# Kernel tuning notes

Measured on AMD Instinct MI355X. Metric: run time of the kernel, lower is better.

Reference implementation:

```python
import jax, jax.numpy as jnp
import numpy as np
from jax import lax

# dims
B, T, D = 2, 1024, 512
H, K, V = 8, 64, 64      # head_k_dim = head_v_dim = 64
CONV = 4
# IVON / module hyperparams (from __init__ defaults)
LR, B1, B2, WD, LAM = 1e-3, 0.9, 0.999, 0.0, 1.0
EPS = 1e-5               # RMSNorm eps
SCALE = K ** -0.5


def _silu(x):
    return x * jax.nn.sigmoid(x)


def _short_conv(x, w):
    """Causal depthwise conv1d (kernel_size=CONV, no bias) + SiLU. x:[B,T,C], w:[C,CONV]."""
    xp = jnp.pad(x, ((0, 0), (CONV - 1, 0), (0, 0)))
    y = sum(xp[:, i:i + x.shape[1]] * w[:, i] for i in range(CONV))
    return _silu(y)


def _l2norm(x):
    return x * lax.rsqrt(jnp.sum(x * x, -1, keepdims=True) + 1e-6)


def setup_inputs() -> dict:
    key = jax.random.key(0)
    ks = jax.random.split(key, 10)
    s = 0.02
    return {
        "hidden_states": jax.random.normal(ks[0], (B, T, D), jnp.float32),
        "Wq": jax.random.normal(ks[1], (D, H * K), jnp.float32) * s,
        "Wk": jax.random.normal(ks[2], (D, H * K), jnp.float32) * s,
        "Wv": jax.random.normal(ks[3], (D, H * V), jnp.float32) * s,
        "Wb": jax.random.normal(ks[4], (D, H), jnp.float32) * s,
        "cw_q": jax.random.normal(ks[5], (H * K, CONV), jnp.float32) * 0.5,
        "cw_k": jax.random.normal(ks[6], (H * K, CONV), jnp.float32) * 0.5,
        "cw_v": jax.random.normal(ks[7], (H * V, CONV), jnp.float32) * 0.5,
        "rms_w": jnp.ones((V,), jnp.float32),
        "Wo": jax.random.normal(ks[8], (H * V, D), jnp.float32) * s,
    }


def reference(hidden_states, Wq, Wk, Wv, Wb, cw_q, cw_k, cw_v, rms_w, Wo):
    x = hidden_states
    # projections -> causal depthwise short conv (+SiLU, qk_activation='silu')
    q = _short_conv(x @ Wq, cw_q).reshape(B, T, H, K)
    k = _short_conv(x @ Wk, cw_k).reshape(B, T, H, K)
    v = _short_conv(x @ Wv, cw_v).reshape(B, T, H, V)
    beta = jax.nn.sigmoid(x @ Wb)                     # [B,T,H]
    # qk l2-norm inside kernel (qk_norm='l2'), scale on q
    q = _l2norm(q) * SCALE
    k = _l2norm(k)

    # fused recurrent IVON delta-rule: per-step outer-product gradient of
    # 0.5||k @ S - v||^2, momentum g, diag preconditioner h (noise-free IVON).
    def step(carry, inp):
        S, h, g = carry                               # each [B,H,K,V]
        qt, kt, vt, bt = inp                          # [B,H,K],[B,H,K],[B,H,V],[B,H]
        pred = jnp.einsum('bhk,bhkv->bhv', kt, S)
        grad = kt[..., None] * (pred - vt)[..., None, :]   # [B,H,K,V]
        g = B1 * g + (1.0 - B1) * grad
        h = B2 * h + (1.0 - B2) * grad * grad
        S = S - LR * bt[..., None, None] * (g + WD * S) / (h + LAM)
        o = jnp.einsum('bhk,bhkv->bhv', qt, S)
        return (S, h, g), o

    z = jnp.zeros((B, H, K, V), jnp.float32)
    inps = (jnp.swapaxes(q, 0, 1), jnp.swapaxes(k, 0, 1),
            jnp.swapaxes(v, 0, 1), jnp.swapaxes(beta, 0, 1))
    _, o = lax.scan(step, (z, z, z), inps)            # o: [T,B,H,V]
    o = jnp.swapaxes(o, 0, 1)                          # [B,T,H,V]

    # RMSNorm over head_v_dim, then output projection
    o = o * lax.rsqrt(jnp.mean(o * o, -1, keepdims=True) + EPS) * rms_w
    o = o.reshape(B, T, H * V) @ Wo                    # [B,T,D]
    return o
```

## Files before the change

kernel.cpp:

```cpp
#include <hip/hip_runtime.h>
#include <hip/hip_bf16.h>
#include <math.h>

#define Bb 2
#define Tt 1024
#define Dd 512
#define Hh 8
#define Kk 64
#define Vv 64
#define BT (Bb*Tt)
#define HK (Hh*Kk)

#define B1c 0.9f
#define B2c 0.999f
#define LRc 1e-3f
#define SCALEc 0.125f

typedef short s8v __attribute__((ext_vector_type(8)));
typedef float f4v __attribute__((ext_vector_type(4)));

__device__ __forceinline__ unsigned short f2bf(float x) {
  unsigned u = __float_as_uint(x);
  u += 0x7FFFu + ((u >> 16) & 1u);
  return (unsigned short)(u >> 16);
}
__device__ __forceinline__ float bf2f(unsigned short h) {
  return __uint_as_float((unsigned)h << 16);
}

template <int CTRL>
__device__ __forceinline__ float dpp_add(float v) {
  int y = __builtin_amdgcn_update_dpp(0, __float_as_int(v), CTRL, 0xF, 0xF, true);
  return v + __int_as_float(y);
}

typedef unsigned uint2_t __attribute__((ext_vector_type(2)));

__device__ __forceinline__ float xor16_add(float x) {
#if __has_builtin(__builtin_amdgcn_permlane16_swap)
  uint2_t r = __builtin_amdgcn_permlane16_swap(__float_as_uint(x), __float_as_uint(x),
                                               false, false);
  return __uint_as_float(r.x) + __uint_as_float(r.y);
#else
  int y = __builtin_amdgcn_ds_swizzle(__float_as_int(x), 0x401F);
  return x + __int_as_float(y);
#endif
}

__device__ __forceinline__ float xor32_add(float x) {
#if __has_builtin(__builtin_amdgcn_permlane32_swap)
  uint2_t r = __builtin_amdgcn_permlane32_swap(__float_as_uint(x), __float_as_uint(x),
                                               false, false);
  return __uint_as_float(r.x) + __uint_as_float(r.y);
#else
  return x + __shfl_xor(x, 32, 64);
#endif
}

__device__ __forceinline__ float reduce16(float x) {
  x = dpp_add<0xB1>(x);
  x = dpp_add<0x4E>(x);
  x = dpp_add<0x141>(x);
  x = dpp_add<0x140>(x);
  return x;
}

__device__ __forceinline__ float reduce64(float x) {
  x = reduce16(x);
  x = xor16_add(x);
  x = xor32_add(x);
  return x;
}

__global__ __launch_bounds__(256) void cvt_x_kernel(
    const float* __restrict__ x, unsigned short* __restrict__ hi,
    unsigned short* __restrict__ lo) {
  const int i = (blockIdx.x * 256 + threadIdx.x) * 8;
  float4 a = *(const float4*)(x + i);
  float4 b = *(const float4*)(x + i + 4);
  const float v[8] = {a.x, a.y, a.z, a.w, b.x, b.y, b.z, b.w};
  union { unsigned short u[8]; uint4 q; } ph, pl;
#pragma unroll
  for (int j = 0; j < 8; ++j) {
    unsigned short h = f2bf(v[j]);
    ph.u[j] = h;
    pl.u[j] = f2bf(v[j] - bf2f(h));
  }
  *(uint4*)(hi + i) = ph.q;
  *(uint4*)(lo + i) = pl.q;
}

__global__ __launch_bounds__(256) void cvt_w_kernel(
    const float* __restrict__ W0, const float* __restrict__ W1,
    const float* __restrict__ W2,
    unsigned short* __restrict__ hib, unsigned short* __restrict__ lob) {
  __shared__ float Ts[64][65];
  const int z = blockIdx.z;
  const float* W = (z == 0) ? W0 : (z == 1) ? W1 : W2;
  unsigned short* hi = hib + (size_t)z * 512 * 512;
  unsigned short* lo = lob + (size_t)z * 512 * 512;
  const int tk = blockIdx.x * 64;
  const int tn = blockIdx.y * 64;
  const int r  = threadIdx.x >> 2;
  const int cg = threadIdx.x & 3;
#pragma unroll
  for (int j = 0; j < 4; ++j) {
    float4 v = *(const float4*)(W + (size_t)(tk + r) * 512 + tn + cg * 16 + j * 4);
    Ts[r][cg * 16 + j * 4 + 0] = v.x;
    Ts[r][cg * 16 + j * 4 + 1] = v.y;
    Ts[r][cg * 16 + j * 4 + 2] = v.z;
    Ts[r][cg * 16 + j * 4 + 3] = v.w;
  }
  __syncthreads();
  union { unsigned short u[16]; uint4 q[2]; } ph, pl;
#pragma unroll
  for (int j = 0; j < 16; ++j) {
    float v = Ts[cg * 16 + j][r];
    unsigned short h = f2bf(v);
    ph.u[j] = h;
    pl.u[j] = f2bf(v - bf2f(h));
  }
  const size_t ob = (size_t)(tn + r) * 512 + tk + cg * 16;
  *(uint4*)(hi + ob) = ph.q[0];
  *(uint4*)(hi + ob + 8) = ph.q[1];
  *(uint4*)(lo + ob) = pl.q[0];
  *(uint4*)(lo + ob + 8) = pl.q[1];
}

__device__ __forceinline__ void gemm_mfma_body(
    const unsigned short* __restrict__ Ahi, const unsigned short* __restrict__ Alo,
    const unsigned short* __restrict__ Bhi, const unsigned short* __restrict__ Blo,
    float* __restrict__ C) {
  __shared__ unsigned short Ah[64][40], Al[64][40], Bh[64][40], Bl[64][40];
  const int tid = threadIdx.x;
  const int bm = blockIdx.x * 64;
  const int bn = blockIdx.y * 64;
  const int srow = tid >> 2;
  const int skoff = (tid & 3) * 8;
  const int l = tid & 63, w = tid >> 6;
  const int arow = (l & 15) + 16 * w;
  const int koff = (l >> 4) * 8;

  const unsigned short* pAh = Ahi + (size_t)(bm + srow) * 512 + skoff;
  const unsigned short* pAl = Alo + (size_t)(bm + srow) * 512 + skoff;
  const unsigned short* pBh = Bhi + (size_t)(bn + srow) * 512 + skoff;
  const unsigned short* pBl = Blo + (size_t)(bn + srow) * 512 + skoff;

  f4v acc0 = {0.f, 0.f, 0.f, 0.f}, acc1 = acc0, acc2 = acc0, acc3 = acc0;

  uint4 rah = *(const uint4*)(pAh);
  uint4 ral = *(const uint4*)(pAl);
  uint4 rbh = *(const uint4*)(pBh);
  uint4 rbl = *(const uint4*)(pBl);

  for (int k0 = 0; k0 < 512; k0 += 32) {
    __syncthreads();
    *(uint4*)&Ah[srow][skoff] = rah;
    *(uint4*)&Al[srow][skoff] = ral;
    *(uint4*)&Bh[srow][skoff] = rbh;
    *(uint4*)&Bl[srow][skoff] = rbl;
    __syncthreads();
    if (k0 + 32 < 512) {
      rah = *(const uint4*)(pAh + k0 + 32);
      ral = *(const uint4*)(pAl + k0 + 32);
      rbh = *(const uint4*)(pBh + k0 + 32);
      rbl = *(const uint4*)(pBl + k0 + 32);
    }
    const s8v ah = *(const s8v*)&Ah[arow][koff];
    const s8v al = *(const s8v*)&Al[arow][koff];
#pragma unroll
    for (int c = 0; c < 4; ++c) {
      const s8v bh = *(const s8v*)&Bh[16 * c + (l & 15)][koff];
      const s8v bl = *(const s8v*)&Bl[16 * c + (l & 15)][koff];
      f4v* acc = (c == 0) ? &acc0 : (c == 1) ? &acc1 : (c == 2) ? &acc2 : &acc3;
      *acc = __builtin_amdgcn_mfma_f32_16x16x32_bf16(al, bh, *acc, 0, 0, 0);
      *acc = __builtin_amdgcn_mfma_f32_16x16x32_bf16(ah, bl, *acc, 0, 0, 0);
      *acc = __builtin_amdgcn_mfma_f32_16x16x32_bf16(ah, bh, *acc, 0, 0, 0);
    }
  }

  const int crow = bm + 16 * w + (l >> 4) * 4;
  const int ccol = bn + (l & 15);
#pragma unroll
  for (int i = 0; i < 4; ++i) {
    C[(size_t)(crow + i) * 512 + ccol + 0]  = acc0[i];
    C[(size_t)(crow + i) * 512 + ccol + 16] = acc1[i];
    C[(size_t)(crow + i) * 512 + ccol + 32] = acc2[i];
    C[(size_t)(crow + i) * 512 + ccol + 48] = acc3[i];
  }
}

__global__ __launch_bounds__(256) void gemm3_mfma_kernel(
    const unsigned short* __restrict__ xhi, const unsigned short* __restrict__ xlo,
    const unsigned short* __restrict__ whi, const unsigned short* __restrict__ wlo,
    float* __restrict__ qp, float* __restrict__ kp, float* __restrict__ vp) {
  const int z = blockIdx.z;
  float* Cp = (z == 0) ? qp : (z == 1) ? kp : vp;
  gemm_mfma_body(xhi, xlo, whi + (size_t)z * 512 * 512, wlo + (size_t)z * 512 * 512, Cp);
}

__global__ __launch_bounds__(256) void gemm1_mfma_kernel(
    const unsigned short* __restrict__ ahi, const unsigned short* __restrict__ alo,
    const unsigned short* __restrict__ whi, const unsigned short* __restrict__ wlo,
    float* __restrict__ C) {
  gemm_mfma_body(ahi, alo, whi, wlo, C);
}

__global__ __launch_bounds__(256) void beta_kernel(const float* __restrict__ x,
                                                   const float* __restrict__ Wb,
                                                   float* __restrict__ beta) {
  int gid = blockIdx.x * blockDim.x + threadIdx.x;
  int bt = gid >> 3, h = gid & 7;
  const float4* xr = (const float4*)(x + (size_t)bt * Dd);
  float s = 0.f;
#pragma unroll 4
  for (int d4 = 0; d4 < Dd / 4; ++d4) {
    float4 xv = xr[d4];
    const float* wb = Wb + (d4 * 4) * Hh + h;
    s = fmaf(xv.x, wb[0 * Hh], s);
    s = fmaf(xv.y, wb[1 * Hh], s);
    s = fmaf(xv.z, wb[2 * Hh], s);
    s = fmaf(xv.w, wb[3 * Hh], s);
  }
  beta[gid] = 1.f / (1.f + expf(-s));
}

__global__ __launch_bounds__(256) void conv_kernel(
    const float* __restrict__ qp, const float* __restrict__ kp,
    const float* __restrict__ vp,
    const float* __restrict__ cwq, const float* __restrict__ cwk,
    const float* __restrict__ cwv,
    float* __restrict__ qc, float* __restrict__ kc, float* __restrict__ vc) {
  const int mode = blockIdx.z;
  const float* pre; const float* cw; float* post;
  if (mode == 0)      { pre = qp; cw = cwq; post = qc; }
  else if (mode == 1) { pre = kp; cw = cwk; post = kc; }
  else                { pre = vp; cw = cwv; post = vc; }

  const int idx = blockIdx.x * 4 + (threadIdx.x >> 6);
  const int lane = threadIdx.x & 63;
  const int b = idx >> 13;
  const int th = idx & 8191;
  const int t = th >> 3;
  const int h = th & 7;
  const int ch = h * 64 + lane;

  float y = 0.f;
#pragma unroll
  for (int i = 0; i < 4; ++i) {
    int tt = t + i - 3;
    if (tt >= 0)
      y += pre[((size_t)(b * Tt + tt)) * HK + ch] * cw[ch * 4 + i];
  }
  y = y / (1.f + expf(-y));
  if (mode < 2) {
    float ss = reduce64(y * y);
    y *= rsqrtf(ss + 1e-6f);
    if (mode == 0) y *= SCALEc;
  }
  post[((size_t)(b * Tt + t)) * HK + ch] = y;
}

#define TC 32

__global__ __launch_bounds__(256) void scan_kernel(
    const float* __restrict__ qc, const float* __restrict__ kc,
    const float* __restrict__ vc, const float* __restrict__ beta,
    float* __restrict__ o) {
  __shared__ float ks[2][TC][64];
  __shared__ float qs[2][TC][64];
  __shared__ float2 vb[2][TC][4];

  const int tid  = threadIdx.x;
  const int lane = tid & 63;
  const int w    = tid >> 6;
  const int bid  = blockIdx.x;
  const int vq   = bid >> 4;
  const int bh   = bid & 15;
  const int b = bh >> 3, h = bh & 7;
  const int v  = vq * 4 + w;

  const size_t base2 = ((size_t)b * Tt) * HK + h * 64;
  const float* bp = beta + ((size_t)b * Tt) * Hh + h;
  float* op = o + base2 + v;

  const int sr = tid >> 4;
  const int sg = tid & 15;
  const int vr = tid >> 3;
  const int vcc = tid & 3;

  {
    float4 k0 = *(const float4*)(kc + base2 + (size_t)sr * HK + sg * 4);
    float4 q0 = *(const float4*)(qc + base2 + (size_t)sr * HK + sg * 4);
    float4 k1 = *(const float4*)(kc + base2 + (size_t)(sr + 16) * HK + sg * 4);
    float4 q1 = *(const float4*)(qc + base2 + (size_t)(sr + 16) * HK + sg * 4);
    *(float4*)&ks[0][sr][sg * 4] = k0;
    *(float4*)&qs[0][sr][sg * 4] = q0;
    *(float4*)&ks[0][sr + 16][sg * 4] = k1;
    *(float4*)&qs[0][sr + 16][sg * 4] = q1;
    if ((tid & 7) < 4) {
      float vv = vc[base2 + (size_t)vr * HK + vq * 4 + vcc];
      float lb = (0.1f * LRc) * bp[(size_t)vr * Hh];
      vb[0][vr][vcc] = make_float2(vv, lb);
    }
    __syncthreads();
  }

  float S = 0.f, G = 0.f, H = 0.f, r = 1.f;

  for (int tile = 0; tile < Tt / TC; ++tile) {
    const int d = tile & 1;
    const int t0 = tile * TC;
    const int more = (tile + 1 < Tt / TC);
    const int tn = more ? t0 + TC : t0;

    float4 nk0 = *(const float4*)(kc + base2 + (size_t)(tn + sr) * HK + sg * 4);
    float4 nq0 = *(const float4*)(qc + base2 + (size_t)(tn + sr) * HK + sg * 4);
    float4 nk1 = *(const float4*)(kc + base2 + (size_t)(tn + sr + 16) * HK + sg * 4);
    float4 nq1 = *(const float4*)(qc + base2 + (size_t)(tn + sr + 16) * HK + sg * 4);
    float nv = 0.f, nb = 0.f;
    if ((tid & 7) < 4) {
      nv = vc[base2 + (size_t)(tn + vr) * HK + vq * 4 + vcc];
      nb = (0.1f * LRc) * bp[(size_t)(tn + vr) * Hh];
    }

    float pred = reduce64(ks[d][0][lane] * S);

#pragma unroll
    for (int s = 0; s < TC; ++s) {
      const float kv = ks[d][s][lane];
      const float qv = qs[d][s][lane];
      const float2 vbc = vb[d][s][w];

      const float diff = pred - vbc.x;
      const float lrb = vbc.y;
      const float gr = kv * diff;
      G = fmaf(B1c, G, gr);
      H = fmaf(B2c, H, gr * gr);
      const float dd = fmaf(H, 0.001f, 1.0f);
      r = r * fmaf(-dd, r, 2.0f);
      S = fmaf(-lrb, G * r, S);

      float po = qv * S;
      if (s + 1 < TC) {
        float pp = ks[d][s + 1][lane] * S;
        po = dpp_add<0xB1>(po);   pp = dpp_add<0xB1>(pp);
        po = dpp_add<0x4E>(po);   pp = dpp_add<0x4E>(pp);
        po = dpp_add<0x141>(po);  pp = dpp_add<0x141>(pp);
        po = dpp_add<0x140>(po);  pp = dpp_add<0x140>(pp);
        po = xor16_add(po);       pp = xor16_add(pp);
        po = xor32_add(po);       pp = xor32_add(pp);
        pred = pp;
      } else {
        po = reduce64(po);
      }
      op[(size_t)(t0 + s) * HK] = po;
    }

    if (more) {
      *(float4*)&ks[d ^ 1][sr][sg * 4] = nk0;
      *(float4*)&qs[d ^ 1][sr][sg * 4] = nq0;
      *(float4*)&ks[d ^ 1][sr + 16][sg * 4] = nk1;
      *(float4*)&qs[d ^ 1][sr + 16][sg * 4] = nq1;
      if ((tid & 7) < 4) vb[d ^ 1][vr][vcc] = make_float2(nv, nb);
    }
    __syncthreads();
  }
}

__global__ __launch_bounds__(256) void rmsnorm_kernel(
    const float* __restrict__ o, const float* __restrict__ rmsw,
    unsigned short* __restrict__ hi, unsigned short* __restrict__ lo) {
  const int idx = blockIdx.x * 4 + (threadIdx.x >> 6);
  const int lane = threadIdx.x & 63;
  const float* p = o + (size_t)idx * 64;
  float y = p[lane];
  float ss = reduce64(y * y);
  y = y * rsqrtf(ss * (1.f / 64.f) + 1e-5f) * rmsw[lane];
  unsigned short h = f2bf(y);
  hi[(size_t)idx * 64 + lane] = h;
  lo[(size_t)idx * 64 + lane] = f2bf(y - bf2f(h));
}

extern "C" void kernel_launch(void* const* d_in, const int* in_sizes, int n_in,
                              void* d_out, int out_size, void* d_ws, size_t ws_size,
                              hipStream_t stream) {
  const float* x    = (const float*)d_in[0];
  const float* Wq   = (const float*)d_in[1];
  const float* Wk   = (const float*)d_in[2];
  const float* Wv   = (const float*)d_in[3];
  const float* Wb   = (const float*)d_in[4];
  const float* cwq  = (const float*)d_in[5];
  const float* cwk  = (const float*)d_in[6];
  const float* cwv  = (const float*)d_in[7];
  const float* rmsw = (const float*)d_in[8];
  const float* Wo   = (const float*)d_in[9];
  float* out = (float*)d_out;
  float* ws  = (float*)d_ws;

  const size_t SZ = (size_t)BT * HK;
  float* qp   = ws;
  float* kp   = ws + 1 * SZ;
  float* vp   = ws + 2 * SZ;
  float* qc   = ws + 3 * SZ;
  float* kc   = ws + 4 * SZ;
  float* vc   = ws + 5 * SZ;
  float* beta = ws + 6 * SZ;
  float* on   = qp;

  unsigned short* xhi  = (unsigned short*)qc;
  unsigned short* xlo  = xhi + SZ;
  unsigned short* wh3  = (unsigned short*)kc;
  unsigned short* wl3  = wh3 + 3 * 512 * 512;
  unsigned short* wohi = (unsigned short*)vc;
  unsigned short* wolo = wohi + 512 * 512;
  unsigned short* onhi = (unsigned short*)kp;
  unsigned short* onlo = (unsigned short*)vp;

  cvt_x_kernel<<<dim3(BT * Dd / (256 * 8)), 256, 0, stream>>>(x, xhi, xlo);
  cvt_w_kernel<<<dim3(8, 8, 3), 256, 0, stream>>>(Wq, Wk, Wv, wh3, wl3);
  gemm3_mfma_kernel<<<dim3(BT / 64, HK / 64, 3), 256, 0, stream>>>(
      xhi, xlo, wh3, wl3, qp, kp, vp);
  beta_kernel<<<dim3(BT * Hh / 256), 256, 0, stream>>>(x, Wb, beta);
  conv_kernel<<<dim3(Bb * Tt * Hh / 4, 1, 3), 256, 0, stream>>>(
      qp, kp, vp, cwq, cwk, cwv, qc, kc, vc);
  scan_kernel<<<dim3(Bb * Hh * (Vv / 4)), 256, 0, stream>>>(
      qc, kc, vc, beta, on);
  cvt_w_kernel<<<dim3(8, 8, 1), 256, 0, stream>>>(Wo, Wo, Wo, wohi, wolo);
  rmsnorm_kernel<<<dim3(Bb * Tt * Hh / 4), 256, 0, stream>>>(on, rmsw, onhi, onlo);
  gemm1_mfma_kernel<<<dim3(BT / 64, HK / 64, 1), 256, 0, stream>>>(
      onhi, onlo, wohi, wolo, out);
}
```

Baseline: 204.4 us.

## Warp-specialize scan: compute waves update state, helper waves load and emit outputs

The scan block grows to 512 threads. Four waves run only the serial recurrence and write each step's state column to a shared buffer. The other four waves prefetch the next tile of q/k/v/beta into a triple-buffered shared area and compute the output dot products q·S for the previous tile, one tile behind. This takes the output reduction and global loads off the serial critical path. The cost is more shared memory, a larger block, and one extra trailing output pass.

```diff
diff --git a/kernel.cpp b/kernel.cpp
--- a/kernel.cpp
+++ b/kernel.cpp
@@ -262,34 +262,35 @@
 }
 
 #define TC 32
-
-__global__ __launch_bounds__(256) void scan_kernel(
+#define NT (Tt / TC)
+
+__global__ __launch_bounds__(512) void scan_kernel(
     const float* __restrict__ qc, const float* __restrict__ kc,
     const float* __restrict__ vc, const float* __restrict__ beta,
     float* __restrict__ o) {
-  __shared__ float ks[2][TC][64];
-  __shared__ float qs[2][TC][64];
-  __shared__ float2 vb[2][TC][4];
+  __shared__ float  ks[3][TC][64];
+  __shared__ float  qs[3][TC][64];
+  __shared__ float2 vb[3][TC][4];
+  __shared__ float  Sb[2][TC][4][64];
 
   const int tid  = threadIdx.x;
   const int lane = tid & 63;
-  const int w    = tid >> 6;
+  const int wave = tid >> 6;
   const int bid  = blockIdx.x;
   const int vq   = bid >> 4;
   const int bh   = bid & 15;
   const int b = bh >> 3, h = bh & 7;
-  const int v  = vq * 4 + w;
 
   const size_t base2 = ((size_t)b * Tt) * HK + h * 64;
   const float* bp = beta + ((size_t)b * Tt) * Hh + h;
-  float* op = o + base2 + v;
-
-  const int sr = tid >> 4;
-  const int sg = tid & 15;
-  const int vr = tid >> 3;
-  const int vcc = tid & 3;
-
-  {
+
+  const int tid2 = tid - 256;
+  const int sr = (tid2 & 255) >> 4;
+  const int sg = tid2 & 15;
+  const int vr = (tid2 & 255) >> 3;
+  const int vcc = tid2 & 3;
+
+  if (wave >= 4) {
     float4 k0 = *(const float4*)(kc + base2 + (size_t)sr * HK + sg * 4);
     float4 q0 = *(const float4*)(qc + base2 + (size_t)sr * HK + sg * 4);
     float4 k1 = *(const float4*)(kc + base2 + (size_t)(sr + 16) * HK + sg * 4);
@@ -298,73 +299,94 @@
     *(float4*)&qs[0][sr][sg * 4] = q0;
     *(float4*)&ks[0][sr + 16][sg * 4] = k1;
     *(float4*)&qs[0][sr + 16][sg * 4] = q1;
-    if ((tid & 7) < 4) {
+    if ((tid2 & 7) < 4) {
       float vv = vc[base2 + (size_t)vr * HK + vq * 4 + vcc];
       float lb = (0.1f * LRc) * bp[(size_t)vr * Hh];
       vb[0][vr][vcc] = make_float2(vv, lb);
     }
-    __syncthreads();
-  }
+  }
+  __syncthreads();
 
   float S = 0.f, G = 0.f, H = 0.f, r = 1.f;
-
-  for (int tile = 0; tile < Tt / TC; ++tile) {
-    const int d = tile & 1;
+  float pred = 0.f;
+
+  int d = 0;
+  for (int tile = 0; tile < NT; ++tile) {
+    const int dn = (d + 1 == 3) ? 0 : d + 1;
+    const int dm = (d == 0) ? 2 : d - 1;
+    const int sb = tile & 1, sbp = sb ^ 1;
     const int t0 = tile * TC;
-    const int more = (tile + 1 < Tt / TC);
-    const int tn = more ? t0 + TC : t0;
-
-    float4 nk0 = *(const float4*)(kc + base2 + (size_t)(tn + sr) * HK + sg * 4);
-    float4 nq0 = *(const float4*)(qc + base2 + (size_t)(tn + sr) * HK + sg * 4);
-    float4 nk1 = *(const float4*)(kc + base2 + (size_t)(tn + sr + 16) * HK + sg * 4);
-    float4 nq1 = *(const float4*)(qc + base2 + (size_t)(tn + sr + 16) * HK + sg * 4);
-    float nv = 0.f, nb = 0.f;
-    if ((tid & 7) < 4) {
-      nv = vc[base2 + (size_t)(tn + vr) * HK + vq * 4 + vcc];
-      nb = (0.1f * LRc) * bp[(size_t)(tn + vr) * Hh];
-    }
-
-    float pred = reduce64(ks[d][0][lane] * S);
-
-#pragma unroll
-    for (int s = 0; s < TC; ++s) {
-      const float kv = ks[d][s][lane];
-      const float qv = qs[d][s][lane];
-      const float2 vbc = vb[d][s][w];
-
-      const float diff = pred - vbc.x;
-      const float lrb = vbc.y;
-      const float gr = kv * diff;
-      G = fmaf(B1c, G, gr);
-      H = fmaf(B2c, H, gr * gr);
-      const float dd = fmaf(H, 0.001f, 1.0f);
-      r = r * fmaf(-dd, r, 2.0f);
-      S = fmaf(-lrb, G * r, S);
-
-      float po = qv * S;
-      if (s + 1 < TC) {
-        float pp = ks[d][s + 1][lane] * S;
-        po = dpp_add<0xB1>(po);   pp = dpp_add<0xB1>(pp);
-        po = dpp_add<0x4E>(po);   pp = dpp_add<0x4E>(pp);
-        po = dpp_add<0x141>(po);  pp = dpp_add<0x141>(pp);
-        po = dpp_add<0x140>(po);  pp = dpp_add<0x140>(pp);
-        po = xor16_add(po);       pp = xor16_add(pp);
-        po = xor32_add(po);       pp = xor32_add(pp);
-        pred = pp;
-      } else {
-        po = reduce64(po);
+    const int more = (tile + 1 < NT);
+
+    if (wave < 4) {
+      const int w = wave;
+      pred = reduce64(ks[d][0][lane] * S);
+#pragma unroll
+      for (int s = 0; s < TC; ++s) {
+        const float kv = ks[d][s][lane];
+        const float2 vbc = vb[d][s][w];
+        const float diff = pred - vbc.x;
+        const float lrb = vbc.y;
+        const float gr = kv * diff;
+        G = fmaf(B1c, G, gr);
+        H = fmaf(B2c, H, gr * gr);
+        const float dd = fmaf(H, 0.001f, 1.0f);
+        r = r * fmaf(-dd, r, 2.0f);
+        S = fmaf(-lrb, G * r, S);
+        Sb[sb][s][w][lane] = S;
+        if (s + 1 < TC)
+          pred = reduce64(ks[d][s + 1][lane] * S);
       }
-      op[(size_t)(t0 + s) * HK] = po;
-    }
-
-    if (more) {
-      *(float4*)&ks[d ^ 1][sr][sg * 4] = nk0;
-      *(float4*)&qs[d ^ 1][sr][sg * 4] = nq0;
-      *(float4*)&ks[d ^ 1][sr + 16][sg * 4] = nk1;
-      *(float4*)&qs[d ^ 1][sr + 16][sg * 4] = nq1;
-      if ((tid & 7) < 4) vb[d ^ 1][vr][vcc] = make_float2(nv, nb);
+    } else {
+      float4 nk0, nq0, nk1, nq1; float nv = 0.f, nb = 0.f;
+      if (more) {
+        const int tn = t0 + TC;
+        nk0 = *(const float4*)(kc + base2 + (size_t)(tn + sr) * HK + sg * 4);
+        nq0 = *(const float4*)(qc + base2 + (size_t)(tn + sr) * HK + sg * 4);
+        nk1 = *(const float4*)(kc + base2 + (size_t)(tn + sr + 16) * HK + sg * 4);
+        nq1 = *(const float4*)(qc + base2 + (size_t)(tn + sr + 16) * HK + sg * 4);
+        if ((tid2 & 7) < 4) {
+          nv = vc[base2 + (size_t)(tn + vr) * HK + vq * 4 + vcc];
+          nb = (0.1f * LRc) * bp[(size_t)(tn + vr) * Hh];
+        }
+      }
+      if (tile > 0) {
+        const int cb = wave - 4;
+        float* opc = o + base2 + vq * 4 + cb;
+        const int tp0 = t0 - TC;
+#pragma unroll
+        for (int s = 0; s < TC; ++s) {
+          const float qv = qs[dm][s][lane];
+          const float Sv = Sb[sbp][s][cb][lane];
+          const float po = reduce64(qv * Sv);
+          opc[(size_t)(tp0 + s) * HK] = po;
+        }
+      }
+      if (more) {
+        *(float4*)&ks[dn][sr][sg * 4] = nk0;
+        *(float4*)&qs[dn][sr][sg * 4] = nq0;
+        *(float4*)&ks[dn][sr + 16][sg * 4] = nk1;
+        *(float4*)&qs[dn][sr + 16][sg * 4] = nq1;
+        if ((tid2 & 7) < 4) vb[dn][vr][vcc] = make_float2(nv, nb);
+      }
     }
     __syncthreads();
+    d = dn;
+  }
+
+  if (wave >= 4) {
+    const int dlast = (NT - 1) % 3;
+    const int sbl = (NT - 1) & 1;
+    const int cb = wave - 4;
+    float* opc = o + base2 + vq * 4 + cb;
+    const int tp0 = (NT - 1) * TC;
+#pragma unroll
+    for (int s = 0; s < TC; ++s) {
+      const float qv = qs[dlast][s][lane];
+      const float Sv = Sb[sbl][s][cb][lane];
+      const float po = reduce64(qv * Sv);
+      opc[(size_t)(tp0 + s) * HK] = po;
+    }
   }
 }
 
@@ -424,7 +446,7 @@
   beta_kernel<<<dim3(BT * Hh / 256), 256, 0, stream>>>(x, Wb, beta);
   conv_kernel<<<dim3(Bb * Tt * Hh / 4, 1, 3), 256, 0, stream>>>(
       qp, kp, vp, cwq, cwk, cwv, qc, kc, vc);
-  scan_kernel<<<dim3(Bb * Hh * (Vv / 4)), 256, 0, stream>>>(
+  scan_kernel<<<dim3(Bb * Hh * (Vv / 4)), 512, 0, stream>>>(
       qc, kc, vc, beta, on);
   cvt_w_kernel<<<dim3(8, 8, 1), 256, 0, stream>>>(Wo, Wo, Wo, wohi, wolo);
   rmsnorm_kernel<<<dim3(Bb * Tt * Hh / 4), 256, 0, stream>>>(on, rmsw, onhi, onlo);
```

Result: faster. 180.4 us, median of 2 (-11.7%).
